# Kernel tuning notes

Measured on AMD Instinct MI355X. Metric: run time of the kernel, lower is better.

The kernel has to match this reference:

```python
import jax, jax.numpy as jnp
import numpy as np

# Dims: B batch, CK key dim, CV value dim, NOBJ objects, T memory frames, HxW feature map
B, CK, CV, NOBJ, T, H, W = 1, 64, 512, 2, 2, 64, 64


def setup_inputs() -> dict:
    key = jax.random.key(0)
    k1, k2, k3, k4, k5 = jax.random.split(key, 5)
    return {
        "query_key": jax.random.normal(k1, (B, CK, H, W), jnp.float32),
        "query_selection": jax.random.uniform(k2, (B, CK, H, W), jnp.float32),
        "memory_key": jax.random.normal(k3, (B, CK, T, H, W), jnp.float32),
        "memory_shrinkage": jax.random.uniform(k4, (B, 1, T, H, W), jnp.float32),
        "memory_value": jax.random.normal(k5, (B, NOBJ, CV, T, H, W), jnp.float32),
    }


def reference(query_key, query_selection, memory_key, memory_shrinkage, memory_value):
    b, nobj, cv = memory_value.shape[:3]
    ck = memory_key.shape[1]
    h, w = query_key.shape[-2:]
    hw = h * w
    mk = memory_key.reshape(b, ck, -1)            # (b, ck, N) with N = T*H*W
    ms = memory_shrinkage.reshape(b, -1)          # (b, N)
    qk = query_key.reshape(b, ck, hw)             # (b, ck, hw)
    qe = query_selection.reshape(b, ck, hw)       # (b, ck, hw)
    mv = memory_value.reshape(b, nobj * cv, -1)   # (b, nobj*cv, N)

    # Negative L2 similarity with selection weighting (XMem get_similarity)
    a_sq = jnp.einsum('bcn,bcp->bnp', mk * mk, qe)            # (b, N, hw)
    two_ab = 2.0 * jnp.einsum('bcn,bcp->bnp', mk, qk * qe)    # (b, N, hw)
    b_sq = jnp.sum(qe * qk * qk, axis=1, keepdims=True)       # (b, 1, hw)
    inv_sqrt_ck = np.float32(1.0 / np.sqrt(ck))
    sim = (two_ab - a_sq - b_sq) * ms[:, :, None] * inv_sqrt_ck

    # Softmax over memory slots (dim N), then weighted readout
    aff = jax.nn.softmax(sim, axis=1)                          # (b, N, hw)
    mem = jnp.einsum('bvn,bnp->bvp', mv, aff)                  # (b, nobj*cv, hw)
    return mem.reshape(b, nobj, cv, h, w)
```

## Files before the change

kernel.cpp:

```cpp
#include <hip/hip_runtime.h>
#include <stdint.h>

typedef unsigned short u16;
typedef __attribute__((ext_vector_type(4))) float f32x4;
typedef __attribute__((ext_vector_type(8))) __bf16 bf16x8;
typedef __attribute__((ext_vector_type(4))) unsigned int u32x4;

#define HWPX 4096
#define NMEM 8192
#define CKD  64
#define VROWS 1024

__device__ __forceinline__ u16 f2bf(float x) {
    union { float f; unsigned u; } v; v.f = x;
    unsigned r = v.u + 0x7FFFu + ((v.u >> 16) & 1u);
    return (u16)(r >> 16);
}

__device__ __forceinline__ void gld_lds16(const void* g, void* l) {
    __builtin_amdgcn_global_load_lds(
        (const __attribute__((address_space(1))) uint32_t*)g,
        (__attribute__((address_space(3))) uint32_t*)l, 16, 0, 0);
}

__global__ void prep_qk(const float* __restrict__ qk, const float* __restrict__ qe,
                        const float* __restrict__ mk,
                        u16* __restrict__ Qhat, float* __restrict__ bsq,
                        u16* __restrict__ Khat) {
    const int bx = blockIdx.x;
    const int tid = threadIdx.x;
    if (bx < 16) {
        int p = bx * 256 + tid;
        float acc = 0.f;
        #pragma unroll 4
        for (int c = 0; c < CKD; ++c) {
            float k = qk[c * HWPX + p];
            float e = qe[c * HWPX + p];
            Qhat[p * 128 + c]      = f2bf(k * e);
            Qhat[p * 128 + 64 + c] = f2bf(e);
            acc += e * k * k;
        }
        bsq[p] = acc;
    } else {
        int n = (bx - 16) * 256 + tid;
        #pragma unroll 4
        for (int c = 0; c < CKD; ++c) {
            float m = mk[c * NMEM + n];
            Khat[n * 128 + c]      = f2bf(2.f * m);
            Khat[n * 128 + 64 + c] = f2bf(-m * m);
        }
    }
}

__launch_bounds__(256, 6)
__global__ void gemm1_combo(const u16* __restrict__ Qhat, const u16* __restrict__ Khat,
                            const float* __restrict__ bsq, const float* __restrict__ ms,
                            const float* __restrict__ mv,
                            u16* __restrict__ Pt, float* __restrict__ dpart,
                            u16* __restrict__ mvb, float* __restrict__ outz) {
    const int blk = blockIdx.x;
    const int tid = threadIdx.x;

    if (blk < 512) {
        #pragma unroll 4
        for (int it = 0; it < 16; ++it) {
            int i = blk * 4096 + it * 256 + tid;
            float4 v = ((const float4*)mv)[i];
            u16 o0 = f2bf(v.x), o1 = f2bf(v.y), o2 = f2bf(v.z), o3 = f2bf(v.w);
            unsigned lo = (unsigned)o0 | ((unsigned)o1 << 16);
            unsigned hi = (unsigned)o2 | ((unsigned)o3 << 16);
            ((uint2*)mvb)[i] = make_uint2(lo, hi);
        }
        return;
    }
    if (blk < 768) {
        #pragma unroll 4
        for (int it = 0; it < 16; ++it) {
            int i = (blk - 512) * 4096 + it * 256 + tid;
            ((float4*)outz)[i] = make_float4(0.f, 0.f, 0.f, 0.f);
        }
        return;
    }

    __shared__ __align__(16) u16 smem[12288];
    u16* Qs = smem;
    u16* Ks = smem + 4096;

    const int tile = blk - 768;
    const int bx = tile & 63;
    const int by = tile >> 6;
    const int p0 = bx * 64;
    const int n0 = by * 128;

    const int l    = tid & 63;
    const int w    = tid >> 6;
    const int quad = l >> 4;
    const int l15  = l & 15;
    const int wm = w >> 1, wn = w & 1;

    const int rsub = tid >> 3;
    const int csw  = (tid & 7) ^ (rsub & 7);

    f32x4 acc[2][4] = {};

    #pragma unroll
    for (int h = 0; h < 2; ++h) {
        if (h) __syncthreads();
        #pragma unroll
        for (int rnd = 0; rnd < 2; ++rnd)
            gld_lds16(Qhat + (size_t)(p0 + rnd * 32 + rsub) * 128 + h * 64 + csw * 8,
                      Qs + rnd * 2048 + w * 512);
        #pragma unroll
        for (int rnd = 0; rnd < 4; ++rnd)
            gld_lds16(Khat + (size_t)(n0 + rnd * 32 + rsub) * 128 + h * 64 + csw * 8,
                      Ks + rnd * 2048 + w * 512);
        __syncthreads();
        #pragma unroll
        for (int kk = 0; kk < 2; ++kk) {
            bf16x8 a[2], b[4];
            #pragma unroll
            for (int mi = 0; mi < 2; ++mi) {
                int row = wm * 32 + mi * 16 + l15;
                a[mi] = *(const bf16x8*)(Qs + row * 64 + (((kk * 4 + quad) ^ (l15 & 7)) << 3));
            }
            #pragma unroll
            for (int ni = 0; ni < 4; ++ni) {
                int row = wn * 64 + ni * 16 + l15;
                b[ni] = *(const bf16x8*)(Ks + row * 64 + (((kk * 4 + quad) ^ (l15 & 7)) << 3));
            }
            #pragma unroll
            for (int mi = 0; mi < 2; ++mi)
                #pragma unroll
                for (int ni = 0; ni < 4; ++ni)
                    acc[mi][ni] = __builtin_amdgcn_mfma_f32_16x16x32_bf16(a[mi], b[ni], acc[mi][ni], 0, 0, 0);
        }
    }

    float msv[4];
    #pragma unroll
    for (int ni = 0; ni < 4; ++ni)
        msv[ni] = ms[n0 + wn * 64 + ni * 16 + l15] * 0.125f;
    float bsv[2][4];
    #pragma unroll
    for (int mi = 0; mi < 2; ++mi)
        #pragma unroll
        for (int r = 0; r < 4; ++r)
            bsv[mi][r] = bsq[p0 + wm * 32 + mi * 16 + quad * 4 + r];

    __syncthreads();
    u16* Ps = smem;
    float rowsum[2][4] = {};
    #pragma unroll
    for (int mi = 0; mi < 2; ++mi) {
        #pragma unroll
        for (int ni = 0; ni < 4; ++ni) {
            f32x4 v = acc[mi][ni];
            int col = wn * 64 + ni * 16 + l15;
            #pragma unroll
            for (int r = 0; r < 4; ++r) {
                int rowl = wm * 32 + mi * 16 + quad * 4 + r;
                float pv = __expf((v[r] - bsv[mi][r]) * msv[ni]);
                rowsum[mi][r] += pv;
                Ps[rowl * 136 + col] = f2bf(pv);
            }
        }
    }
    #pragma unroll
    for (int mi = 0; mi < 2; ++mi)
        #pragma unroll
        for (int r = 0; r < 4; ++r) {
            float s = rowsum[mi][r];
            s += __shfl_xor(s, 1);
            s += __shfl_xor(s, 2);
            s += __shfl_xor(s, 4);
            s += __shfl_xor(s, 8);
            rowsum[mi][r] = s;
        }
    if (l15 < 8) {
        float myv = 0.f;
        #pragma unroll
        for (int mi = 0; mi < 2; ++mi)
            #pragma unroll
            for (int r = 0; r < 4; ++r)
                if (l15 == mi * 4 + r) myv = rowsum[mi][r];
        int slice = by * 2 + wn;
        dpart[(size_t)slice * HWPX + p0 + wm * 32 + (l15 >> 2) * 16 + quad * 4 + (l15 & 3)] = myv;
    }
    __syncthreads();

    {
        const int pb = bx >> 1;
        const size_t dstBase = ((size_t)pb * 64 + by) * 16384 + (size_t)(bx & 1) * 8192;
        #pragma unroll
        for (int i = 0; i < 4; ++i) {
            int row = i * 16 + (tid >> 4);
            const u32x4* src = (const u32x4*)(Ps + row * 136 + (tid & 15) * 8);
            u32x4* dst = (u32x4*)(Pt + dstBase + i * 2048 + tid * 8);
            *dst = *src;
        }
    }
}

__launch_bounds__(256, 4)
__global__ void gemm2_kernel(const u16* __restrict__ Ab, const u16* __restrict__ Bt,
                             const float* __restrict__ dpart, float* __restrict__ outacc) {
    __shared__ __align__(16) u16 As[128 * 64];
    __shared__ __align__(16) u16 Bs[128 * 64];

    const int tid  = threadIdx.x;
    const int l    = tid & 63;
    const int w    = tid >> 6;
    const int quad = l >> 4;
    const int l15  = l & 15;
    const int wm = w >> 1, wn = w & 1;

    const int lin = blockIdx.x + (blockIdx.y << 3) + (blockIdx.z << 8);
    const int vb  = (lin >> 3) & 7;
    const int pb  = (lin & 7) | (((lin >> 6) & 3) << 3);
    const int kz  = lin >> 8;
    const int v0 = vb * 128;
    const int p0 = pb * 128;
    const int kbeg = kz * (NMEM / 4);
    const int kend = kbeg + (NMEM / 4);

    const int rsub = tid >> 3;
    const int csw  = (tid & 7) ^ (rsub & 7);

    f32x4 acc[4][4] = {};

    for (int k0 = kbeg; k0 < kend; k0 += 64) {
        const int nb = k0 >> 7;
        const int nh = (k0 >> 6) & 1;
        const u16* bsrc = Bt + ((size_t)pb * 64 + nb) * 16384 + nh * 64;
        __syncthreads();
        #pragma unroll
        for (int rnd = 0; rnd < 4; ++rnd) {
            gld_lds16(Ab + (size_t)(v0 + rnd * 32 + rsub) * NMEM + k0 + csw * 8,
                      As + rnd * 2048 + w * 512);
            gld_lds16(bsrc + (rnd * 32 + rsub) * 128 + csw * 8,
                      Bs + rnd * 2048 + w * 512);
        }
        __syncthreads();
        #pragma unroll
        for (int kk = 0; kk < 2; ++kk) {
            bf16x8 a[4], b[4];
            #pragma unroll
            for (int mi = 0; mi < 4; ++mi) {
                int row = wm * 64 + mi * 16 + l15;
                a[mi] = *(const bf16x8*)(As + row * 64 + (((kk * 4 + quad) ^ (l15 & 7)) << 3));
            }
            #pragma unroll
            for (int ni = 0; ni < 4; ++ni) {
                int row = wn * 64 + ni * 16 + l15;
                b[ni] = *(const bf16x8*)(Bs + row * 64 + (((kk * 4 + quad) ^ (l15 & 7)) << 3));
            }
            #pragma unroll
            for (int mi = 0; mi < 4; ++mi)
                #pragma unroll
                for (int ni = 0; ni < 4; ++ni)
                    acc[mi][ni] = __builtin_amdgcn_mfma_f32_16x16x32_bf16(a[mi], b[ni], acc[mi][ni], 0, 0, 0);
        }
    }

    __syncthreads();
    float* dtmp = (float*)As;
    float* dinvs = (float*)Bs;
    {
        int p = tid & 127, h = tid >> 7;
        float s = 0.f;
        #pragma unroll 8
        for (int sl = 0; sl < 64; ++sl)
            s += dpart[(size_t)(h * 64 + sl) * HWPX + p0 + p];
        dtmp[tid] = s;
    }
    __syncthreads();
    if (tid < 128) dinvs[tid] = 1.0f / (dtmp[tid] + dtmp[tid + 128]);
    __syncthreads();

    float dinv[4];
    #pragma unroll
    for (int ni = 0; ni < 4; ++ni)
        dinv[ni] = dinvs[wn * 64 + ni * 16 + l15];

    #pragma unroll
    for (int mi = 0; mi < 4; ++mi) {
        #pragma unroll
        for (int ni = 0; ni < 4; ++ni) {
            int col = p0 + wn * 64 + ni * 16 + l15;
            f32x4 v = acc[mi][ni];
            #pragma unroll
            for (int r = 0; r < 4; ++r) {
                int row = v0 + wm * 64 + mi * 16 + quad * 4 + r;
                atomicAdd(&outacc[(size_t)row * HWPX + col], v[r] * dinv[ni]);
            }
        }
    }
}

extern "C" void kernel_launch(void* const* d_in, const int* in_sizes, int n_in,
                              void* d_out, int out_size, void* d_ws, size_t ws_size,
                              hipStream_t stream) {
    const float* qk = (const float*)d_in[0];
    const float* qe = (const float*)d_in[1];
    const float* mk = (const float*)d_in[2];
    const float* ms = (const float*)d_in[3];
    const float* mv = (const float*)d_in[4];
    float* out = (float*)d_out;

    char* ws = (char*)d_ws;
    u16*   Pt    = (u16*)ws;
    u16*   mvb   = (u16*)(ws + ((size_t)64 << 20));
    u16*   Khat  = (u16*)(ws + ((size_t)80 << 20));
    u16*   Qhat  = (u16*)(ws + ((size_t)82 << 20));
    float* bsq   = (float*)(ws + ((size_t)83 << 20));
    float* dpart = (float*)(ws + ((size_t)83 << 20) + 65536);

    prep_qk<<<48, 256, 0, stream>>>(qk, qe, mk, Qhat, bsq, Khat);

    gemm1_combo<<<4864, 256, 0, stream>>>(Qhat, Khat, bsq, ms, mv, Pt, dpart, mvb, out);

    dim3 g2(8, 32, 4);
    gemm2_kernel<<<g2, 256, 0, stream>>>(mvb, Pt, dpart, out);
}
```

Measured before the change: 226.7 us.

## Restructure gemm2 into 512-thread 256x128 tiles with triple-buffered async LDS pipeline

Rewrites the value-readout GEMM as 512-thread blocks with 8 waves covering a 256x128 output tile, split-K reduced from 4 to 2. Global-to-LDS loads go through a three-slot rotating buffer staged two iterations ahead. Each step interleaves partial LDS fragment reads with quadrant MFMA groups under raised wave priority, with explicit vmcnt waits. This aims to hide memory latency behind compute and halve the atomic output traffic. In exchange occupancy drops to two blocks per CU, there are more barriers per iteration, and correctness depends on hand-placed waitcnt counts.

```diff
diff --git a/kernel.cpp b/kernel.cpp
--- a/kernel.cpp
+++ b/kernel.cpp
@@ -201,80 +201,162 @@
     }
 }
 
-__launch_bounds__(256, 4)
+__launch_bounds__(512, 2)
 __global__ void gemm2_kernel(const u16* __restrict__ Ab, const u16* __restrict__ Bt,
                              const float* __restrict__ dpart, float* __restrict__ outacc) {
-    __shared__ __align__(16) u16 As[128 * 64];
-    __shared__ __align__(16) u16 Bs[128 * 64];
+    __shared__ __align__(16) u16 smem[3 * 24576];
 
     const int tid  = threadIdx.x;
     const int l    = tid & 63;
     const int w    = tid >> 6;
     const int quad = l >> 4;
     const int l15  = l & 15;
-    const int wm = w >> 1, wn = w & 1;
-
-    const int lin = blockIdx.x + (blockIdx.y << 3) + (blockIdx.z << 8);
-    const int vb  = (lin >> 3) & 7;
-    const int pb  = (lin & 7) | (((lin >> 6) & 3) << 3);
-    const int kz  = lin >> 8;
-    const int v0 = vb * 128;
-    const int p0 = pb * 128;
-    const int kbeg = kz * (NMEM / 4);
-    const int kend = kbeg + (NMEM / 4);
+    const int wm = w >> 1;
+    const int wn = w & 1;
+
+    const int lin = blockIdx.x;
+    const int xcd = lin & 7;
+    const int PB  = lin >> 3;
+    const int vb  = xcd >> 1;
+    const int kz  = xcd & 1;
+    const int v0 = vb * 256;
+    const int p0 = PB * 128;
+    const int kbeg = kz * (NMEM / 2);
+    const int NT = (NMEM / 2) / 64;
 
     const int rsub = tid >> 3;
     const int csw  = (tid & 7) ^ (rsub & 7);
 
+    u16* pR = smem;
+    u16* pN = smem + 24576;
+    u16* pS = smem + 2 * 24576;
+
+    #define STAGE_A2(n0g, dst, r0)                                                  \
+        { _Pragma("unroll")                                                         \
+          for (int rnd = (r0); rnd < (r0) + 2; ++rnd)                               \
+              gld_lds16(Ab + (size_t)(v0 + rnd * 64 + rsub) * NMEM + (n0g) + csw * 8, \
+                        (dst) + rnd * 4096 + w * 512); }
+    #define STAGE_B(n0g, dst)                                                       \
+        { const int nb_ = (n0g) >> 7, nh_ = ((n0g) >> 6) & 1;                       \
+          const u16* bsrc_ = Bt + ((size_t)PB * 64 + nb_) * 16384 + nh_ * 64;       \
+          _Pragma("unroll")                                                         \
+          for (int rnd = 0; rnd < 2; ++rnd)                                         \
+              gld_lds16(bsrc_ + (rnd * 64 + rsub) * 128 + csw * 8,                  \
+                        (dst) + 16384 + rnd * 4096 + w * 512); }
+
+    STAGE_A2(kbeg, pR, 0) STAGE_A2(kbeg, pR, 2) STAGE_B(kbeg, pR)
+    STAGE_A2(kbeg + 64, pN, 0) STAGE_A2(kbeg + 64, pN, 2) STAGE_B(kbeg + 64, pN)
+    asm volatile("s_waitcnt vmcnt(6)" ::: "memory");
+    __builtin_amdgcn_s_barrier();
+
     f32x4 acc[4][4] = {};
 
-    for (int k0 = kbeg; k0 < kend; k0 += 64) {
-        const int nb = k0 >> 7;
-        const int nh = (k0 >> 6) & 1;
-        const u16* bsrc = Bt + ((size_t)pb * 64 + nb) * 16384 + nh * 64;
-        __syncthreads();
-        #pragma unroll
-        for (int rnd = 0; rnd < 4; ++rnd) {
-            gld_lds16(Ab + (size_t)(v0 + rnd * 32 + rsub) * NMEM + k0 + csw * 8,
-                      As + rnd * 2048 + w * 512);
-            gld_lds16(bsrc + (rnd * 32 + rsub) * 128 + csw * 8,
-                      Bs + rnd * 2048 + w * 512);
-        }
-        __syncthreads();
-        #pragma unroll
-        for (int kk = 0; kk < 2; ++kk) {
-            bf16x8 a[4], b[4];
-            #pragma unroll
-            for (int mi = 0; mi < 4; ++mi) {
-                int row = wm * 64 + mi * 16 + l15;
-                a[mi] = *(const bf16x8*)(As + row * 64 + (((kk * 4 + quad) ^ (l15 & 7)) << 3));
-            }
-            #pragma unroll
-            for (int ni = 0; ni < 4; ++ni) {
-                int row = wn * 64 + ni * 16 + l15;
-                b[ni] = *(const bf16x8*)(Bs + row * 64 + (((kk * 4 + quad) ^ (l15 & 7)) << 3));
-            }
-            #pragma unroll
-            for (int mi = 0; mi < 4; ++mi)
+    for (int t = 0; t < NT; ++t) {
+        const bool st = (t < NT - 2);
+        const int n2 = kbeg + (t + 2) * 64;
+        bf16x8 a[4][2], b[4][2];
+
+        #pragma unroll
+        for (int mi = 0; mi < 2; ++mi) {
+            const int row = wm * 64 + mi * 16 + l15;
+            #pragma unroll
+            for (int kk = 0; kk < 2; ++kk)
+                a[mi][kk] = *(const bf16x8*)(pR + row * 64 + (((kk * 4 + quad) ^ (l15 & 7)) << 3));
+        }
+        #pragma unroll
+        for (int ni = 0; ni < 2; ++ni) {
+            const int row = wn * 64 + ni * 16 + l15;
+            #pragma unroll
+            for (int kk = 0; kk < 2; ++kk)
+                b[ni][kk] = *(const bf16x8*)(pR + 16384 + row * 64 + (((kk * 4 + quad) ^ (l15 & 7)) << 3));
+        }
+        if (st) STAGE_A2(n2, pS, 0)
+        __builtin_amdgcn_s_barrier();
+        asm volatile("s_waitcnt lgkmcnt(0)");
+        __builtin_amdgcn_sched_barrier(0);
+        __builtin_amdgcn_s_setprio(1);
+        #pragma unroll
+        for (int mi = 0; mi < 2; ++mi)
+            #pragma unroll
+            for (int ni = 0; ni < 2; ++ni)
                 #pragma unroll
-                for (int ni = 0; ni < 4; ++ni)
-                    acc[mi][ni] = __builtin_amdgcn_mfma_f32_16x16x32_bf16(a[mi], b[ni], acc[mi][ni], 0, 0, 0);
-        }
-    }
+                for (int kk = 0; kk < 2; ++kk)
+                    acc[mi][ni] = __builtin_amdgcn_mfma_f32_16x16x32_bf16(a[mi][kk], b[ni][kk], acc[mi][ni], 0, 0, 0);
+        __builtin_amdgcn_s_setprio(0);
+        __builtin_amdgcn_s_barrier();
+
+        #pragma unroll
+        for (int ni = 2; ni < 4; ++ni) {
+            const int row = wn * 64 + ni * 16 + l15;
+            #pragma unroll
+            for (int kk = 0; kk < 2; ++kk)
+                b[ni][kk] = *(const bf16x8*)(pR + 16384 + row * 64 + (((kk * 4 + quad) ^ (l15 & 7)) << 3));
+        }
+        if (st) STAGE_A2(n2, pS, 2)
+        __builtin_amdgcn_s_barrier();
+        asm volatile("s_waitcnt lgkmcnt(0)");
+        __builtin_amdgcn_sched_barrier(0);
+        __builtin_amdgcn_s_setprio(1);
+        #pragma unroll
+        for (int mi = 0; mi < 2; ++mi)
+            #pragma unroll
+            for (int ni = 2; ni < 4; ++ni)
+                #pragma unroll
+                for (int kk = 0; kk < 2; ++kk)
+                    acc[mi][ni] = __builtin_amdgcn_mfma_f32_16x16x32_bf16(a[mi][kk], b[ni][kk], acc[mi][ni], 0, 0, 0);
+        __builtin_amdgcn_s_setprio(0);
+        __builtin_amdgcn_s_barrier();
+
+        #pragma unroll
+        for (int mi = 2; mi < 4; ++mi) {
+            const int row = wm * 64 + mi * 16 + l15;
+            #pragma unroll
+            for (int kk = 0; kk < 2; ++kk)
+                a[mi][kk] = *(const bf16x8*)(pR + row * 64 + (((kk * 4 + quad) ^ (l15 & 7)) << 3));
+        }
+        if (st) STAGE_B(n2, pS)
+        __builtin_amdgcn_s_barrier();
+        asm volatile("s_waitcnt lgkmcnt(0)");
+        __builtin_amdgcn_sched_barrier(0);
+        __builtin_amdgcn_s_setprio(1);
+        #pragma unroll
+        for (int mi = 2; mi < 4; ++mi)
+            #pragma unroll
+            for (int ni = 2; ni < 4; ++ni)
+                #pragma unroll
+                for (int kk = 0; kk < 2; ++kk)
+                    acc[mi][ni] = __builtin_amdgcn_mfma_f32_16x16x32_bf16(a[mi][kk], b[ni][kk], acc[mi][ni], 0, 0, 0);
+        #pragma unroll
+        for (int mi = 2; mi < 4; ++mi)
+            #pragma unroll
+            for (int ni = 0; ni < 2; ++ni)
+                #pragma unroll
+                for (int kk = 0; kk < 2; ++kk)
+                    acc[mi][ni] = __builtin_amdgcn_mfma_f32_16x16x32_bf16(a[mi][kk], b[ni][kk], acc[mi][ni], 0, 0, 0);
+        __builtin_amdgcn_s_setprio(0);
+
+        if (t < NT - 2) { asm volatile("s_waitcnt vmcnt(6)" ::: "memory"); }
+        else            { asm volatile("s_waitcnt vmcnt(0)" ::: "memory"); }
+        __builtin_amdgcn_s_barrier();
+        u16* tmp = pR; pR = pN; pN = pS; pS = tmp;
+    }
+    #undef STAGE_A2
+    #undef STAGE_B
 
     __syncthreads();
-    float* dtmp = (float*)As;
-    float* dinvs = (float*)Bs;
+    float* dtmp  = (float*)smem;
+    float* dinvs = (float*)(smem + 4096);
     {
         int p = tid & 127, h = tid >> 7;
         float s = 0.f;
         #pragma unroll 8
-        for (int sl = 0; sl < 64; ++sl)
-            s += dpart[(size_t)(h * 64 + sl) * HWPX + p0 + p];
+        for (int sl = 0; sl < 32; ++sl)
+            s += dpart[(size_t)(h * 32 + sl) * HWPX + p0 + p];
         dtmp[tid] = s;
     }
     __syncthreads();
-    if (tid < 128) dinvs[tid] = 1.0f / (dtmp[tid] + dtmp[tid + 128]);
+    if (tid < 128)
+        dinvs[tid] = 1.0f / (dtmp[tid] + dtmp[tid + 128] + dtmp[tid + 256] + dtmp[tid + 384]);
     __syncthreads();
 
     float dinv[4];
@@ -319,6 +401,5 @@
 
     gemm1_combo<<<4864, 256, 0, stream>>>(Qhat, Khat, bsq, ms, mv, Pt, dpart, mvb, out);
 
-    dim3 g2(8, 32, 4);
-    gemm2_kernel<<<g2, 256, 0, stream>>>(mvb, Pt, dpart, out);
-}
+    gemm2_kernel<<<256, 512, 0, stream>>>(mvb, Pt, dpart, out);
+}
```

Measured after the change: 217.7 us. -4.0%, faster.

## Software-pipeline gemm2 with 4-stage LDS ring for B and register-prefetched A

Applied to the files above, without the earlier changes.

Rewrites the gemm2 main loop as a software pipeline. B tiles are staged into a 4-deep LDS ring two iterations ahead with direct global-to-LDS loads. A fragments are loaded straight from global memory into registers one iteration ahead, with one barrier per step and raised wave priority around the MFMA block. The K split drops from 4 to 2, giving 512 blocks, and launch bounds are lowered to 2 blocks per CU. This aims to hide memory latency and remove a barrier pair per step, at the cost of more registers, more LDS, fewer blocks and uncoalesced per-lane global A loads.

```diff
diff --git a/kernel.cpp b/kernel.cpp
--- a/kernel.cpp
+++ b/kernel.cpp
@@ -201,70 +201,106 @@
     }
 }
 
-__launch_bounds__(256, 4)
+__launch_bounds__(256, 2)
 __global__ void gemm2_kernel(const u16* __restrict__ Ab, const u16* __restrict__ Bt,
                              const float* __restrict__ dpart, float* __restrict__ outacc) {
-    __shared__ __align__(16) u16 As[128 * 64];
-    __shared__ __align__(16) u16 Bs[128 * 64];
+    __shared__ __align__(16) u16 smem[4 * 8192];
 
     const int tid  = threadIdx.x;
     const int l    = tid & 63;
     const int w    = tid >> 6;
     const int quad = l >> 4;
     const int l15  = l & 15;
-    const int wm = w >> 1, wn = w & 1;
-
-    const int lin = blockIdx.x + (blockIdx.y << 3) + (blockIdx.z << 8);
-    const int vb  = (lin >> 3) & 7;
-    const int pb  = (lin & 7) | (((lin >> 6) & 3) << 3);
-    const int kz  = lin >> 8;
+    const int wm = w >> 1;
+    const int wn = w & 1;
+
+    const int lin  = blockIdx.x;
+    const int vbkz = lin & 15;
+    const int pb   = lin >> 4;
+    const int vb   = vbkz >> 1;
+    const int kz   = vbkz & 1;
     const int v0 = vb * 128;
     const int p0 = pb * 128;
-    const int kbeg = kz * (NMEM / 4);
-    const int kend = kbeg + (NMEM / 4);
+    const int kbeg = kz * (NMEM / 2);
+    const int NT = (NMEM / 2) / 64;
 
     const int rsub = tid >> 3;
     const int csw  = (tid & 7) ^ (rsub & 7);
 
+    const u16* aRow0 = Ab + (size_t)(v0 + wm * 64 +  0 + l15) * NMEM + quad * 8;
+    const u16* aRow1 = Ab + (size_t)(v0 + wm * 64 + 16 + l15) * NMEM + quad * 8;
+    const u16* aRow2 = Ab + (size_t)(v0 + wm * 64 + 32 + l15) * NMEM + quad * 8;
+    const u16* aRow3 = Ab + (size_t)(v0 + wm * 64 + 48 + l15) * NMEM + quad * 8;
+
+    const int c0 = ((0 + quad) ^ (l15 & 7)) << 3;
+    const int c1 = ((4 + quad) ^ (l15 & 7)) << 3;
+    const int bOff = (wn * 64 + l15) * 64;
+
+    #define LOAD_A(dst, ko)                                                      \
+        { dst[0][0] = *(const bf16x8*)(aRow0 + (ko));                            \
+          dst[0][1] = *(const bf16x8*)(aRow0 + (ko) + 32);                       \
+          dst[1][0] = *(const bf16x8*)(aRow1 + (ko));                            \
+          dst[1][1] = *(const bf16x8*)(aRow1 + (ko) + 32);                       \
+          dst[2][0] = *(const bf16x8*)(aRow2 + (ko));                            \
+          dst[2][1] = *(const bf16x8*)(aRow2 + (ko) + 32);                       \
+          dst[3][0] = *(const bf16x8*)(aRow3 + (ko));                            \
+          dst[3][1] = *(const bf16x8*)(aRow3 + (ko) + 32); }
+
+    #define STAGE_B(n0g, dst)                                                    \
+        { const int nb_ = (n0g) >> 7, nh_ = ((n0g) >> 6) & 1;                    \
+          const u16* bsrc_ = Bt + ((size_t)pb * 64 + nb_) * 16384 + nh_ * 64;    \
+          _Pragma("unroll")                                                      \
+          for (int rnd = 0; rnd < 4; ++rnd)                                      \
+              gld_lds16(bsrc_ + (rnd * 32 + rsub) * 128 + csw * 8,               \
+                        (dst) + rnd * 2048 + w * 512); }
+
     f32x4 acc[4][4] = {};
-
-    for (int k0 = kbeg; k0 < kend; k0 += 64) {
-        const int nb = k0 >> 7;
-        const int nh = (k0 >> 6) & 1;
-        const u16* bsrc = Bt + ((size_t)pb * 64 + nb) * 16384 + nh * 64;
-        __syncthreads();
-        #pragma unroll
-        for (int rnd = 0; rnd < 4; ++rnd) {
-            gld_lds16(Ab + (size_t)(v0 + rnd * 32 + rsub) * NMEM + k0 + csw * 8,
-                      As + rnd * 2048 + w * 512);
-            gld_lds16(bsrc + (rnd * 32 + rsub) * 128 + csw * 8,
-                      Bs + rnd * 2048 + w * 512);
-        }
-        __syncthreads();
-        #pragma unroll
-        for (int kk = 0; kk < 2; ++kk) {
-            bf16x8 a[4], b[4];
-            #pragma unroll
-            for (int mi = 0; mi < 4; ++mi) {
-                int row = wm * 64 + mi * 16 + l15;
-                a[mi] = *(const bf16x8*)(As + row * 64 + (((kk * 4 + quad) ^ (l15 & 7)) << 3));
-            }
-            #pragma unroll
-            for (int ni = 0; ni < 4; ++ni) {
-                int row = wn * 64 + ni * 16 + l15;
-                b[ni] = *(const bf16x8*)(Bs + row * 64 + (((kk * 4 + quad) ^ (l15 & 7)) << 3));
-            }
-            #pragma unroll
-            for (int mi = 0; mi < 4; ++mi)
-                #pragma unroll
-                for (int ni = 0; ni < 4; ++ni)
-                    acc[mi][ni] = __builtin_amdgcn_mfma_f32_16x16x32_bf16(a[mi], b[ni], acc[mi][ni], 0, 0, 0);
-        }
-    }
-
-    __syncthreads();
-    float* dtmp = (float*)As;
-    float* dinvs = (float*)Bs;
+    bf16x8 aC[4][2], aN[4][2];
+
+    LOAD_A(aC, kbeg)
+    STAGE_B(kbeg, smem)
+    STAGE_B(kbeg + 64, smem + 8192)
+    asm volatile("s_waitcnt vmcnt(4)" ::: "memory");
+    __builtin_amdgcn_s_barrier();
+    __builtin_amdgcn_sched_barrier(0);
+
+    #define BODY(T, AC, AN)                                                      \
+    {   const int t_ = (T);                                                      \
+        const u16* bufR = smem + ((t_ & 3) * 8192);                              \
+        bf16x8 bfr[4][2];                                                        \
+        _Pragma("unroll")                                                        \
+        for (int ni = 0; ni < 4; ++ni) {                                         \
+            bfr[ni][0] = *(const bf16x8*)(bufR + bOff + ni * 1024 + c0);         \
+            bfr[ni][1] = *(const bf16x8*)(bufR + bOff + ni * 1024 + c1);         \
+        }                                                                        \
+        if (t_ + 1 < NT) LOAD_A(AN, kbeg + (t_ + 1) * 64)                        \
+        if (t_ + 2 < NT) STAGE_B(kbeg + (t_ + 2) * 64, smem + (((t_ + 2) & 3) * 8192)) \
+        __builtin_amdgcn_s_setprio(1);                                           \
+        _Pragma("unroll")                                                        \
+        for (int mi = 0; mi < 4; ++mi)                                           \
+            _Pragma("unroll")                                                    \
+            for (int ni = 0; ni < 4; ++ni) {                                     \
+                acc[mi][ni] = __builtin_amdgcn_mfma_f32_16x16x32_bf16(AC[mi][0], bfr[ni][0], acc[mi][ni], 0, 0, 0); \
+                acc[mi][ni] = __builtin_amdgcn_mfma_f32_16x16x32_bf16(AC[mi][1], bfr[ni][1], acc[mi][ni], 0, 0, 0); \
+            }                                                                    \
+        __builtin_amdgcn_s_setprio(0);                                           \
+        if (t_ + 2 < NT) { asm volatile("s_waitcnt vmcnt(4)" ::: "memory"); }    \
+        else             { asm volatile("s_waitcnt vmcnt(0)" ::: "memory"); }    \
+        __builtin_amdgcn_s_barrier();                                            \
+        __builtin_amdgcn_sched_barrier(0);                                       \
+    }
+
+    for (int tt = 0; tt < NT; tt += 2) {
+        BODY(tt, aC, aN)
+        BODY(tt + 1, aN, aC)
+    }
+    #undef BODY
+    #undef STAGE_B
+    #undef LOAD_A
+
+    __syncthreads();
+    float* dtmp  = (float*)smem;
+    float* dinvs = (float*)(smem + 2048);
     {
         int p = tid & 127, h = tid >> 7;
         float s = 0.f;
@@ -319,6 +355,5 @@
 
     gemm1_combo<<<4864, 256, 0, stream>>>(Qhat, Khat, bsq, ms, mv, Pt, dpart, mvb, out);
 
-    dim3 g2(8, 32, 4);
-    gemm2_kernel<<<g2, 256, 0, stream>>>(mvb, Pt, dpart, out);
-}
+    gemm2_kernel<<<512, 256, 0, stream>>>(mvb, Pt, dpart, out);
+}
```

Result: slower. 276.7 us (+22.1%).
